# Performance work log

Measured on AMD Instinct MI355X. Metric: run time of the kernel, lower is better.

Reference implementation:

```python
import jax, jax.numpy as jnp
import numpy as np

D = 300      # dim_in (hardcoded in HGConv)
N_CAT = 3    # n_categories
M = 16384    # nodes
E = 4096     # hyperedges


def setup_inputs() -> dict:
    key = jax.random.key(0)
    ks = jax.random.split(key, 11)
    s = 1.0 / np.sqrt(D)
    u = lambda k, shape: jax.random.uniform(k, shape, jnp.float32, -s, s)
    return {
        "node_feats": jax.random.normal(ks[0], (M, D), jnp.float32),
        "edge_feats": jax.random.normal(ks[1], (E, D), jnp.float32),
        "inc_mat": jax.random.uniform(ks[2], (M, E), jnp.float32),
        # VertexConv params (Linear weights stored as (in, out); torch stores transpose)
        "W_att": u(ks[3], (D, D)),       # attention, no bias
        "W_proj": u(ks[4], (D, D)),      # projection, no bias
        "alpha": jnp.array(0.5, jnp.float32),
        # HypergraphEdgeAggregation params
        "ec_W_att": u(ks[5], (D, 1)),    # attention, no bias
        "ec_W_proj": u(ks[6], (D, D)),
        "ec_b_proj": u(ks[7], (D,)),
        # final classifier
        "fc_W": u(ks[8], (D, N_CAT)),
        "fc_b": u(ks[9], (N_CAT,)),
    }


def reference(node_feats, edge_feats, inc_mat, W_att, W_proj, alpha,
              ec_W_att, ec_W_proj, ec_b_proj, fc_W, fc_b):
    # --- VertexConv ---
    # edge attention scores: inc^T @ (X @ W_att)  -> (e, d)
    edge_att = inc_mat.T @ (node_feats @ W_att)
    attn = jax.nn.softmax(edge_att, axis=1)
    # fused equivalent of einsum('me,md->med') then einsum('med,ed->ed'):
    # edge_feat[e,d] = (inc^T @ X)[e,d] * attn[e,d]
    ef = (inc_mat.T @ node_feats) * attn
    ef = ef @ W_proj
    ef = alpha * edge_feats + (1.0 - alpha) * ef          # residual mix
    # --- HypergraphEdgeAggregation ---
    scores = ef @ ec_W_att                                # (e, 1)
    w = jax.nn.softmax(scores, axis=0)                    # softmax over edges
    pooled = jnp.sum(ef * w, axis=0)                      # (d,)
    out = pooled @ ec_W_proj + ec_b_proj                  # (d,)
    # --- classifier (LogSoftmax is defined but NOT applied in forward) ---
    logits = out @ fc_W + fc_b                            # (n_categories,)
    return logits
```

## Files before the change

### kernel.cpp

```cpp
#include <hip/hip_runtime.h>
#include <math.h>

typedef _Float16 f16;
typedef _Float16 f16x8 __attribute__((ext_vector_type(8)));
typedef _Float16 f16x4 __attribute__((ext_vector_type(4)));
typedef __fp16 fp16x2 __attribute__((ext_vector_type(2)));
typedef float f32x4 __attribute__((ext_vector_type(4)));
typedef float f32x16 __attribute__((ext_vector_type(16)));

#define NM 16384
#define NE 4096
#define ND 300
#define DP 320
#define PS 1310720

__device__ __forceinline__ int swz(int r) { return (r ^ (r >> 2)) & 3; }

#define GLOAD_LDS16(gsrc, ldst)                                              \
  __builtin_amdgcn_global_load_lds(                                          \
      (__attribute__((address_space(1))) void*)(gsrc),                       \
      (__attribute__((address_space(3))) void*)(ldst), 16, 0, 0)

__global__ __launch_bounds__(256) void k01_prep(const float* __restrict__ X,
                                                const float* __restrict__ Watt,
                                                f16* __restrict__ XT,
                                                f16* __restrict__ WT) {
  __shared__ f16 tile[64][324];
  const int bx = blockIdx.x;
  if (bx < 256) {
    int m0 = bx * 64;
    for (int idx = threadIdx.x; idx < 64 * 80; idx += 256) {
      int m = idx / 80, q = idx % 80;
      int d = q * 4;
      float4 v = make_float4(0.f, 0.f, 0.f, 0.f);
      if (d < ND) v = *(const float4*)(X + (size_t)(m0 + m) * ND + d);
      tile[m][d] = (f16)v.x; tile[m][d + 1] = (f16)v.y;
      tile[m][d + 2] = (f16)v.z; tile[m][d + 3] = (f16)v.w;
    }
    __syncthreads();
    for (int idx = threadIdx.x; idx < DP * 8; idx += 256) {
      int d = idx >> 3, part = idx & 7;
      f16x8 hv;
#pragma unroll
      for (int i = 0; i < 8; ++i) hv[i] = tile[part * 8 + i][d];
      *(f16x8*)(XT + (size_t)d * NM + m0 + part * 8) = hv;
    }
  } else {
    int idx = (bx - 256) * 256 + threadIdx.x;
    if (idx < DP * DP) {
      int j = idx / DP, d = idx % DP;
      float v = (j < ND && d < ND) ? Watt[d * ND + j] : 0.f;
      WT[(size_t)j * DP + d] = (f16)v;
    }
  }
}

#define K2WAIT(N) asm volatile("s_waitcnt vmcnt(" #N ") lgkmcnt(0)" ::: "memory")
#define K2BAR()                                        \
  do {                                                 \
    asm volatile("" ::: "memory");                     \
    __builtin_amdgcn_s_barrier();                      \
    asm volatile("" ::: "memory");                     \
  } while (0)

__global__ __launch_bounds__(256, 2) void k2_bigmm(const float* __restrict__ inc,
                                                   const f16* __restrict__ XT,
                                                   f16* __restrict__ Zp) {
  __shared__ __align__(16) char lds[57344];
  const int t = threadIdx.x, lane = t & 63, wid = t >> 6;
  const int bx = blockIdx.x;
  const int kb = (bx & 7) | (((bx >> 3) & 1) << 3);
  const int eb = bx >> 4;
  const int e0 = eb * 128;
  const size_t kbase = (size_t)kb * 1024;
  f16* __restrict__ Zout = Zp + (size_t)kb * PS;

  const int we = wid >> 1, wj = wid & 1;
  const int l31 = lane & 31, oct = lane >> 5;
  int sl[2];
#pragma unroll
  for (int kk = 0; kk < 2; ++kk)
    sl[kk] = (((kk * 2 + oct) ^ ((l31 >> 1) & 3)) & 3) << 4;
  const int arow = (we * 64 + l31) * 64;
  const int brow = (wj * 160 + l31) * 64;
  const int ep = t & 63, kq = t >> 6;
  const int sA = (kq ^ ((ep >> 1) & 3)) & 3;
  const int wa0 = 40960 + ep * 64 + sA * 16;
  const int wa1 = 40960 + (ep + 64) * 64 + sA * 16;
  const float* pA = inc + (kbase + kq * 8) * NE + e0 + ep;
  const int br = wid * 80 + (lane >> 2);
  const f16* pB = XT + (size_t)br * NM + kbase + 8 * ((lane & 3) ^ ((lane >> 3) & 3));

  float rAx0[8], rAy0[8], rAx1[8], rAy1[8];
  f32x16 acc[2][5];
#pragma unroll
  for (int me = 0; me < 2; ++me)
#pragma unroll
    for (int f = 0; f < 5; ++f)
#pragma unroll
      for (int r = 0; r < 16; ++r) acc[me][f][r] = 0.f;

#define LOADA(RX, RY)                                                          \
  {                                                                            \
    _Pragma("unroll") for (int i = 0; i < 8; ++i) {                            \
      RX[i] = pA[(size_t)i * NE];                                              \
      RY[i] = pA[(size_t)i * NE + 64];                                         \
    }                                                                          \
    pA += (size_t)32 * NE;                                                     \
  }
#define DMAB(S)                                                                \
  {                                                                            \
    _Pragma("unroll") for (int i = 0; i < 5; ++i) {                            \
      GLOAD_LDS16(pB + (size_t)(i * 16) * NM,                                  \
                  lds + (S)*20480 + wid * 5120 + i * 1024);                    \
    }                                                                          \
    pB += 32;                                                                  \
  }
#define WRITEA(RX, RY, S)                                                      \
  {                                                                            \
    union { fp16x2 h; uint32_t u; } ux_[4], uy_[4];                            \
    _Pragma("unroll") for (int z = 0; z < 4; ++z) {                            \
      ux_[z].h = __builtin_amdgcn_cvt_pkrtz(RX[2 * z], RX[2 * z + 1]);         \
      uy_[z].h = __builtin_amdgcn_cvt_pkrtz(RY[2 * z], RY[2 * z + 1]);         \
    }                                                                          \
    *(uint4*)(lds + wa0 + (S)*8192) =                                          \
        make_uint4(ux_[0].u, ux_[1].u, ux_[2].u, ux_[3].u);                    \
    *(uint4*)(lds + wa1 + (S)*8192) =                                          \
        make_uint4(uy_[0].u, uy_[1].u, uy_[2].u, uy_[3].u);                    \
  }
#define COMPUTE(S)                                                             \
  {                                                                            \
    __builtin_amdgcn_s_setprio(1);                                             \
    _Pragma("unroll") for (int kk = 0; kk < 2; ++kk) {                         \
      f16x8 a0_ = *(const f16x8*)(lds + 40960 + (S)*8192 + arow + sl[kk]);     \
      f16x8 a1_ = *(const f16x8*)(lds + 40960 + (S)*8192 + arow + 2048 + sl[kk]); \
      _Pragma("unroll") for (int f = 0; f < 5; ++f) {                          \
        f16x8 b_ = *(const f16x8*)(lds + (S)*20480 + brow + f * 2048 + sl[kk]); \
        acc[0][f] = __builtin_amdgcn_mfma_f32_32x32x16_f16(a0_, b_, acc[0][f], 0, 0, 0); \
        acc[1][f] = __builtin_amdgcn_mfma_f32_32x32x16_f16(a1_, b_, acc[1][f], 0, 0, 0); \
      }                                                                        \
    }                                                                          \
    __builtin_amdgcn_s_setprio(0);                                             \
  }

  LOADA(rAx0, rAy0);
  DMAB(0);
  WRITEA(rAx0, rAy0, 0);
  LOADA(rAx0, rAy0);
  DMAB(1);
  K2WAIT(21);
  K2BAR();

  for (int it = 0; it < 15; ++it) {
    COMPUTE(0);
    K2BAR();
    LOADA(rAx1, rAy1);
    DMAB(0);
    WRITEA(rAx0, rAy0, 1);
    K2WAIT(21);
    K2BAR();
    COMPUTE(1);
    K2BAR();
    LOADA(rAx0, rAy0);
    DMAB(1);
    WRITEA(rAx1, rAy1, 0);
    K2WAIT(21);
    K2BAR();
  }
  COMPUTE(0);
  K2BAR();
  WRITEA(rAx0, rAy0, 1);
  K2WAIT(0);
  K2BAR();
  COMPUTE(1);

#pragma unroll
  for (int me = 0; me < 2; ++me)
#pragma unroll
    for (int f = 0; f < 5; ++f) {
      int jg = wj * 160 + f * 32 + l31;
      int ebase = e0 + we * 64 + me * 32 + 4 * oct;
#pragma unroll
      for (int r = 0; r < 16; ++r) {
        int eg = ebase + (r & 3) + 8 * (r >> 2);
        Zout[(size_t)eg * DP + jg] = (f16)acc[me][f][r];
      }
    }
#undef LOADA
#undef DMAB
#undef WRITEA
}

__global__ __launch_bounds__(256) void k2s_sum(const f16* __restrict__ Zp,
                                               f16* __restrict__ EF0) {
  const int idx = (blockIdx.x * 256 + threadIdx.x) * 4;
  float s0 = 0.f, s1 = 0.f, s2 = 0.f, s3 = 0.f;
#pragma unroll
  for (int i = 0; i < 16; ++i) {
    f16x4 v = *(const f16x4*)(Zp + (size_t)i * PS + idx);
    s0 += (float)v[0]; s1 += (float)v[1]; s2 += (float)v[2]; s3 += (float)v[3];
  }
  f16x4 o;
  o[0] = (f16)s0; o[1] = (f16)s1; o[2] = (f16)s2; o[3] = (f16)s3;
  *(f16x4*)(EF0 + idx) = o;
}

__global__ __launch_bounds__(256, 1) void k2b_att(const f16* __restrict__ EF0,
                                                  const f16* __restrict__ WT,
                                                  float* __restrict__ att) {
  constexpr int STEPS = 10;
  __shared__ __align__(16) char lds[57344];
  const int t = threadIdx.x, lane = t & 63, wid = t >> 6;
  const int e0 = blockIdx.x * 128;
  const int we = wid >> 1, wj = wid & 1;
  const int l31 = lane & 31, oct = lane >> 5;
  int sl[2];
#pragma unroll
  for (int kk = 0; kk < 2; ++kk)
    sl[kk] = (((kk * 2 + oct) ^ ((l31 >> 1) & 3)) & 3) << 4;
  const int arow = (we * 64 + l31) * 64;
  const int brow = (wj * 160 + l31) * 64;
  const int srcsw = 8 * ((lane & 3) ^ ((lane >> 3) & 3));
  const f16* pA = EF0 + (size_t)(e0 + wid * 32 + (lane >> 2)) * DP + srcsw;
  const f16* pB = WT + (size_t)(wid * 80 + (lane >> 2)) * DP + srcsw;

  f32x16 acc[2][5];
#pragma unroll
  for (int me = 0; me < 2; ++me)
#pragma unroll
    for (int f = 0; f < 5; ++f)
#pragma unroll
      for (int r = 0; r < 16; ++r) acc[me][f][r] = 0.f;

#define STAGE2(S)                                                              \
  {                                                                            \
    _Pragma("unroll") for (int i = 0; i < 2; ++i) {                            \
      GLOAD_LDS16(pA + (size_t)(i * 16) * DP,                                  \
                  lds + 40960 + (S)*8192 + wid * 2048 + i * 1024);             \
    }                                                                          \
    pA += 32;                                                                  \
    _Pragma("unroll") for (int i = 0; i < 5; ++i) {                            \
      GLOAD_LDS16(pB + (size_t)(i * 16) * DP,                                  \
                  lds + (S)*20480 + wid * 5120 + i * 1024);                    \
    }                                                                          \
    pB += 32;                                                                  \
  }

  STAGE2(0);
  STAGE2(1);
  K2WAIT(7);
  K2BAR();
  for (int tt = 0; tt < STEPS - 2; ++tt) {
    COMPUTE(tt & 1);
    K2BAR();
    STAGE2(tt & 1);
    K2WAIT(7);
    K2BAR();
  }
  COMPUTE(0);
  K2BAR();
  K2WAIT(0);
  COMPUTE(1);

#pragma unroll
  for (int me = 0; me < 2; ++me)
#pragma unroll
    for (int f = 0; f < 5; ++f) {
      int jg = wj * 160 + f * 32 + l31;
      int ebase = e0 + we * 64 + me * 32 + 4 * oct;
#pragma unroll
      for (int r = 0; r < 16; ++r) {
        int eg = ebase + (r & 3) + 8 * (r >> 2);
        att[(size_t)eg * DP + jg] = acc[me][f][r];
      }
    }
#undef STAGE2
#undef COMPUTE
}

__global__ __launch_bounds__(256) void k3_edge(const float* __restrict__ att,
                                               const f16* __restrict__ EF0,
                                               const float* __restrict__ edge_feats,
                                               const float* __restrict__ Wproj,
                                               const float* __restrict__ alphaP,
                                               const float* __restrict__ ecWatt,
                                               float* __restrict__ ef,
                                               float* __restrict__ scores) {
  __shared__ float efw[16][304];
  const int t = threadIdx.x, lane = t & 63, w = t >> 6;
  const int e0 = blockIdx.x * 16;
  for (int el = 0; el < 4; ++el) {
    int e = e0 + w * 4 + el;
    const size_t ro = (size_t)e * DP;
    float p[5];
    float mx = -1e30f;
#pragma unroll
    for (int u = 0; u < 5; ++u) {
      int d = u * 64 + lane;
      p[u] = (d < ND) ? att[ro + d] : -1e30f;
      mx = fmaxf(mx, p[u]);
    }
    for (int o = 32; o; o >>= 1) mx = fmaxf(mx, __shfl_xor(mx, o));
    float s = 0.f;
#pragma unroll
    for (int u = 0; u < 5; ++u) {
      int d = u * 64 + lane;
      float pe = (d < ND) ? expf(p[u] - mx) : 0.f;
      p[u] = pe;
      s += pe;
    }
    for (int o = 32; o; o >>= 1) s += __shfl_xor(s, o);
    float inv = 1.f / s;
#pragma unroll
    for (int u = 0; u < 5; ++u) {
      int d = u * 64 + lane;
      if (d < 304)
        efw[w * 4 + el][d] = (d < ND) ? (float)EF0[ro + d] * p[u] * inv : 0.f;
    }
  }
  __syncthreads();
  const int jl = lane & 15, kc = lane >> 4;
  const float alpha = alphaP[0];
  float acc[4][19];
#pragma unroll
  for (int ei = 0; ei < 4; ++ei)
#pragma unroll
    for (int jj = 0; jj < 19; ++jj) acc[ei][jj] = 0.f;
  const int d0 = kc * 75;
  const float* efw0 = &efw[w * 4 + 0][0];
  const float* efw1 = &efw[w * 4 + 1][0];
  const float* efw2 = &efw[w * 4 + 2][0];
  const float* efw3 = &efw[w * 4 + 3][0];
  for (int dd = 0; dd < 75; ++dd) {
    int d = d0 + dd;
    const float* wr = Wproj + (size_t)d * ND + jl;
    float w0 = efw0[d], w1 = efw1[d], w2 = efw2[d], w3 = efw3[d];
#pragma unroll
    for (int jj = 0; jj < 19; ++jj) {
      int j = jl + jj * 16;
      float wv = (j < ND) ? wr[jj * 16] : 0.f;
      acc[0][jj] += w0 * wv;
      acc[1][jj] += w1 * wv;
      acc[2][jj] += w2 * wv;
      acc[3][jj] += w3 * wv;
    }
  }
#pragma unroll
  for (int ei = 0; ei < 4; ++ei)
#pragma unroll
    for (int jj = 0; jj < 19; ++jj) {
      acc[ei][jj] += __shfl_xor(acc[ei][jj], 16);
      acc[ei][jj] += __shfl_xor(acc[ei][jj], 32);
    }
  float scp[4] = {0.f, 0.f, 0.f, 0.f};
#pragma unroll
  for (int ei = 0; ei < 4; ++ei) {
    int e = e0 + w * 4 + ei;
#pragma unroll
    for (int jj = 0; jj < 19; ++jj) {
      int j = jl + jj * 16;
      float v = 0.f;
      if (j < ND) {
        v = alpha * edge_feats[(size_t)e * ND + j] + (1.f - alpha) * acc[ei][jj];
        scp[ei] += v * ecWatt[j];
      }
      if (kc == 0) ef[(size_t)e * 304 + j] = v;
    }
  }
#pragma unroll
  for (int ei = 0; ei < 4; ++ei)
    for (int o = 8; o; o >>= 1) scp[ei] += __shfl_xor(scp[ei], o);
  if (lane == 0) {
#pragma unroll
    for (int ei = 0; ei < 4; ++ei) scores[e0 + w * 4 + ei] = scp[ei];
  }
}

__global__ __launch_bounds__(256) void k4ab_pool(const float* __restrict__ sc,
                                                 const float* __restrict__ ef,
                                                 float* __restrict__ pp) {
  __shared__ float redm[4];
  __shared__ float reds[4];
  __shared__ float wsh[64];
  const int t = threadIdx.x, lane = t & 63, w = t >> 6;
  float v[16];
  float mx = -1e30f;
#pragma unroll
  for (int u = 0; u < 16; ++u) {
    v[u] = sc[t + u * 256];
    mx = fmaxf(mx, v[u]);
  }
  for (int o = 32; o; o >>= 1) mx = fmaxf(mx, __shfl_xor(mx, o));
  if (lane == 0) redm[w] = mx;
  __syncthreads();
  float m2 = fmaxf(fmaxf(redm[0], redm[1]), fmaxf(redm[2], redm[3]));
  float s = 0.f;
#pragma unroll
  for (int u = 0; u < 16; ++u) s += expf(v[u] - m2);
  for (int o = 32; o; o >>= 1) s += __shfl_xor(s, o);
  if (lane == 0) reds[w] = s;
  __syncthreads();
  float inv = 1.f / (reds[0] + reds[1] + reds[2] + reds[3]);
  const int e0 = blockIdx.x * 64;
  if (t < 64) wsh[t] = expf(sc[e0 + t] - m2) * inv;
  __syncthreads();
  for (int j = t; j < 304; j += 256) {
    float acc = 0.f;
#pragma unroll 8
    for (int e = 0; e < 64; ++e) acc += wsh[e] * ef[(size_t)(e0 + e) * 304 + j];
    pp[blockIdx.x * 304 + j] = acc;
  }
}

__global__ __launch_bounds__(320) void k4c_final(const float* __restrict__ pp,
                                                 const float* __restrict__ ecWp,
                                                 const float* __restrict__ ecb,
                                                 const float* __restrict__ fcW,
                                                 const float* __restrict__ fcb,
                                                 float* __restrict__ out) {
  __shared__ float pooled[304];
  __shared__ float o[304];
  const int t = threadIdx.x;
  if (t < 304) {
    float acc = 0.f;
#pragma unroll 8
    for (int b = 0; b < 64; ++b) acc += pp[b * 304 + t];
    pooled[t] = acc;
  }
  __syncthreads();
  if (t < ND) {
    float acc = ecb[t];
#pragma unroll 4
    for (int j = 0; j < ND; ++j) acc += pooled[j] * ecWp[(size_t)j * ND + t];
    o[t] = acc;
  }
  __syncthreads();
  if (t < 64) {
#pragma unroll
    for (int c = 0; c < 3; ++c) {
      float a = 0.f;
      for (int j2 = t; j2 < ND; j2 += 64) a += o[j2] * fcW[j2 * 3 + c];
      for (int off = 32; off; off >>= 1) a += __shfl_xor(a, off);
      if (t == 0) out[c] = a + fcb[c];
    }
  }
}

extern "C" void kernel_launch(void* const* d_in, const int* in_sizes, int n_in,
                              void* d_out, int out_size, void* d_ws, size_t ws_size,
                              hipStream_t stream) {
  const float* X = (const float*)d_in[0];
  const float* EFEATS = (const float*)d_in[1];
  const float* INC = (const float*)d_in[2];
  const float* WATT = (const float*)d_in[3];
  const float* WPROJ = (const float*)d_in[4];
  const float* ALPHA = (const float*)d_in[5];
  const float* ECATT = (const float*)d_in[6];
  const float* ECWP = (const float*)d_in[7];
  const float* ECB = (const float*)d_in[8];
  const float* FCW = (const float*)d_in[9];
  const float* FCB = (const float*)d_in[10];

  char* ws = (char*)d_ws;
  f16* XT = (f16*)(ws);
  f16* Zp = (f16*)(ws + 10485760);
  f16* WT = (f16*)(ws + 52428800);
  f16* EF0 = (f16*)(ws + 52633600);
  float* att = (float*)(ws + 55255040);
  float* ef = (float*)(ws + 60497920);
  float* sc = (float*)(ws + 65478656);
  float* pp = (float*)(ws + 65495040);

  hipLaunchKernelGGL(k01_prep, dim3(656), dim3(256), 0, stream, X, WATT, XT, WT);
  hipLaunchKernelGGL(k2_bigmm, dim3(512), dim3(256), 0, stream, INC, XT, Zp);
  hipLaunchKernelGGL(k2s_sum, dim3(1280), dim3(256), 0, stream, Zp, EF0);
  hipLaunchKernelGGL(k2b_att, dim3(32), dim3(256), 0, stream, EF0, WT, att);
  hipLaunchKernelGGL(k3_edge, dim3(256), dim3(256), 0, stream, att, EF0, EFEATS,
                     WPROJ, ALPHA, ECATT, ef, sc);
  hipLaunchKernelGGL(k4ab_pool, dim3(64), dim3(256), 0, stream, sc, ef, pp);
  hipLaunchKernelGGL(k4c_final, dim3(1), dim3(320), 0, stream, pp, ECWP, ECB, FCW,
                     FCB, (float*)d_out);
}
```

Before: 245.1 us.

## Triple-buffer big GEMM B tiles, vectorize A loads, fuse split-K sum into attention GEMM

```diff
diff --git a/kernel.cpp b/kernel.cpp
--- a/kernel.cpp
+++ b/kernel.cpp
@@ -14,12 +14,24 @@
 #define DP 320
 #define PS 1310720
 
-__device__ __forceinline__ int swz(int r) { return (r ^ (r >> 2)) & 3; }
-
 #define GLOAD_LDS16(gsrc, ldst)                                              \
   __builtin_amdgcn_global_load_lds(                                          \
       (__attribute__((address_space(1))) void*)(gsrc),                       \
       (__attribute__((address_space(3))) void*)(ldst), 16, 0, 0)
+
+#define K2WAIT(N) asm volatile("s_waitcnt vmcnt(" #N ") lgkmcnt(0)" ::: "memory")
+#define K2BAR()                                        \
+  do {                                                 \
+    asm volatile("" ::: "memory");                     \
+    __builtin_amdgcn_s_barrier();                      \
+    asm volatile("" ::: "memory");                     \
+  } while (0)
+#define K2BARW()                                       \
+  do {                                                 \
+    asm volatile("s_waitcnt lgkmcnt(0)" ::: "memory"); \
+    __builtin_amdgcn_s_barrier();                      \
+    asm volatile("" ::: "memory");                     \
+  } while (0)
 
 __global__ __launch_bounds__(256) void k01_prep(const float* __restrict__ X,
                                                 const float* __restrict__ Watt,
@@ -55,18 +67,10 @@
   }
 }
 
-#define K2WAIT(N) asm volatile("s_waitcnt vmcnt(" #N ") lgkmcnt(0)" ::: "memory")
-#define K2BAR()                                        \
-  do {                                                 \
-    asm volatile("" ::: "memory");                     \
-    __builtin_amdgcn_s_barrier();                      \
-    asm volatile("" ::: "memory");                     \
-  } while (0)
-
 __global__ __launch_bounds__(256, 2) void k2_bigmm(const float* __restrict__ inc,
                                                    const f16* __restrict__ XT,
                                                    f16* __restrict__ Zp) {
-  __shared__ __align__(16) char lds[57344];
+  __shared__ __align__(16) char lds[77824];
   const int t = threadIdx.x, lane = t & 63, wid = t >> 6;
   const int bx = blockIdx.x;
   const int kb = (bx & 7) | (((bx >> 3) & 1) << 3);
@@ -84,14 +88,13 @@
   const int arow = (we * 64 + l31) * 64;
   const int brow = (wj * 160 + l31) * 64;
   const int ep = t & 63, kq = t >> 6;
-  const int sA = (kq ^ ((ep >> 1) & 3)) & 3;
-  const int wa0 = 40960 + ep * 64 + sA * 16;
-  const int wa1 = 40960 + (ep + 64) * 64 + sA * 16;
-  const float* pA = inc + (kbase + kq * 8) * NE + e0 + ep;
+  const int sA = (kq ^ (ep & 3)) & 3;
+  const int wa0 = 61440 + ep * 128 + sA * 16;
+  const float* pA = inc + (kbase + kq * 8) * NE + e0 + 2 * ep;
   const int br = wid * 80 + (lane >> 2);
   const f16* pB = XT + (size_t)br * NM + kbase + 8 * ((lane & 3) ^ ((lane >> 3) & 3));
 
-  float rAx0[8], rAy0[8], rAx1[8], rAy1[8];
+  float2 rA0[8], rA1[8];
   f32x16 acc[2][5];
 #pragma unroll
   for (int me = 0; me < 2; ++me)
@@ -100,12 +103,10 @@
 #pragma unroll
       for (int r = 0; r < 16; ++r) acc[me][f][r] = 0.f;
 
-#define LOADA(RX, RY)                                                          \
-  {                                                                            \
-    _Pragma("unroll") for (int i = 0; i < 8; ++i) {                            \
-      RX[i] = pA[(size_t)i * NE];                                              \
-      RY[i] = pA[(size_t)i * NE + 64];                                         \
-    }                                                                          \
+#define LOADA(R)                                                               \
+  {                                                                            \
+    _Pragma("unroll") for (int i = 0; i < 8; ++i)                              \
+        R[i] = *(const float2*)(pA + (size_t)i * NE);                          \
     pA += (size_t)32 * NE;                                                     \
   }
 #define DMAB(S)                                                                \
@@ -116,63 +117,66 @@
     }                                                                          \
     pB += 32;                                                                  \
   }
-#define WRITEA(RX, RY, S)                                                      \
+#define WRITEA(R, S)                                                           \
   {                                                                            \
     union { fp16x2 h; uint32_t u; } ux_[4], uy_[4];                            \
     _Pragma("unroll") for (int z = 0; z < 4; ++z) {                            \
-      ux_[z].h = __builtin_amdgcn_cvt_pkrtz(RX[2 * z], RX[2 * z + 1]);         \
-      uy_[z].h = __builtin_amdgcn_cvt_pkrtz(RY[2 * z], RY[2 * z + 1]);         \
+      ux_[z].h = __builtin_amdgcn_cvt_pkrtz(R[2 * z].x, R[2 * z + 1].x);       \
+      uy_[z].h = __builtin_amdgcn_cvt_pkrtz(R[2 * z].y, R[2 * z + 1].y);       \
     }                                                                          \
     *(uint4*)(lds + wa0 + (S)*8192) =                                          \
         make_uint4(ux_[0].u, ux_[1].u, ux_[2].u, ux_[3].u);                    \
-    *(uint4*)(lds + wa1 + (S)*8192) =                                          \
+    *(uint4*)(lds + wa0 + 64 + (S)*8192) =                                     \
         make_uint4(uy_[0].u, uy_[1].u, uy_[2].u, uy_[3].u);                    \
   }
-#define COMPUTE(S)                                                             \
+#define COMPUTE(BS, AS)                                                        \
   {                                                                            \
     __builtin_amdgcn_s_setprio(1);                                             \
     _Pragma("unroll") for (int kk = 0; kk < 2; ++kk) {                         \
-      f16x8 a0_ = *(const f16x8*)(lds + 40960 + (S)*8192 + arow + sl[kk]);     \
-      f16x8 a1_ = *(const f16x8*)(lds + 40960 + (S)*8192 + arow + 2048 + sl[kk]); \
+      f16x8 a0_ = *(const f16x8*)(lds + 61440 + (AS)*8192 + arow + sl[kk]);    \
+      f16x8 a1_ = *(const f16x8*)(lds + 61440 + (AS)*8192 + arow + 2048 + sl[kk]); \
       _Pragma("unroll") for (int f = 0; f < 5; ++f) {                          \
-        f16x8 b_ = *(const f16x8*)(lds + (S)*20480 + brow + f * 2048 + sl[kk]); \
+        f16x8 b_ = *(const f16x8*)(lds + (BS)*20480 + brow + f * 2048 + sl[kk]); \
         acc[0][f] = __builtin_amdgcn_mfma_f32_32x32x16_f16(a0_, b_, acc[0][f], 0, 0, 0); \
         acc[1][f] = __builtin_amdgcn_mfma_f32_32x32x16_f16(a1_, b_, acc[1][f], 0, 0, 0); \
       }                                                                        \
     }                                                                          \
     __builtin_amdgcn_s_setprio(0);                                             \
   }
-
-  LOADA(rAx0, rAy0);
+#define BODY(BSTG, BCMP, AW, AC, RL, RW)                                       \
+  DMAB(BSTG);                                                                  \
+  LOADA(RL);                                                                   \
+  WRITEA(RW, AW); \
+  K2BARW();                                                                    \
+  COMPUTE(BCMP, AC);                                                           \
+  K2BAR();
+
+  LOADA(rA0);
   DMAB(0);
-  WRITEA(rAx0, rAy0, 0);
-  LOADA(rAx0, rAy0);
+  WRITEA(rA0, 0);
+  LOADA(rA1);
   DMAB(1);
-  K2WAIT(21);
-  K2BAR();
-
-  for (int it = 0; it < 15; ++it) {
-    COMPUTE(0);
-    K2BAR();
-    LOADA(rAx1, rAy1);
-    DMAB(0);
-    WRITEA(rAx0, rAy0, 1);
-    K2WAIT(21);
-    K2BAR();
-    COMPUTE(1);
-    K2BAR();
-    LOADA(rAx0, rAy0);
-    DMAB(1);
-    WRITEA(rAx1, rAy1, 0);
-    K2WAIT(21);
-    K2BAR();
-  }
-  COMPUTE(0);
-  K2BAR();
-  WRITEA(rAx0, rAy0, 1);
+  BODY(2, 0, 1, 0, rA0, rA1);
+
+  for (int it = 0; it < 4; ++it) {
+    BODY(0, 1, 0, 1, rA1, rA0);
+    BODY(1, 2, 1, 0, rA0, rA1);
+    BODY(2, 0, 0, 1, rA1, rA0);
+    BODY(0, 1, 1, 0, rA0, rA1);
+    BODY(1, 2, 0, 1, rA1, rA0);
+    BODY(2, 0, 1, 0, rA0, rA1);
+  }
+  BODY(0, 1, 0, 1, rA1, rA0);
+  BODY(1, 2, 1, 0, rA0, rA1);
+  BODY(2, 0, 0, 1, rA1, rA0);
+  BODY(0, 1, 1, 0, rA0, rA1);
+  BODY(1, 2, 0, 1, rA1, rA0);
+  WRITEA(rA1, 1);
   K2WAIT(0);
   K2BAR();
-  COMPUTE(1);
+  COMPUTE(0, 0);
+  K2BAR();
+  COMPUTE(1, 1);
 
 #pragma unroll
   for (int me = 0; me < 2; ++me)
@@ -189,55 +193,59 @@
 #undef LOADA
 #undef DMAB
 #undef WRITEA
-}
-
-__global__ __launch_bounds__(256) void k2s_sum(const f16* __restrict__ Zp,
-                                               f16* __restrict__ EF0) {
-  const int idx = (blockIdx.x * 256 + threadIdx.x) * 4;
-  float s0 = 0.f, s1 = 0.f, s2 = 0.f, s3 = 0.f;
-#pragma unroll
-  for (int i = 0; i < 16; ++i) {
-    f16x4 v = *(const f16x4*)(Zp + (size_t)i * PS + idx);
-    s0 += (float)v[0]; s1 += (float)v[1]; s2 += (float)v[2]; s3 += (float)v[3];
-  }
-  f16x4 o;
-  o[0] = (f16)s0; o[1] = (f16)s1; o[2] = (f16)s2; o[3] = (f16)s3;
-  *(f16x4*)(EF0 + idx) = o;
-}
-
-__global__ __launch_bounds__(256, 1) void k2b_att(const f16* __restrict__ EF0,
-                                                  const f16* __restrict__ WT,
-                                                  float* __restrict__ att) {
-  constexpr int STEPS = 10;
-  __shared__ __align__(16) char lds[57344];
+#undef COMPUTE
+#undef BODY
+}
+
+__global__ __launch_bounds__(256, 1) void k2bs_att(const f16* __restrict__ Zp,
+                                                   const f16* __restrict__ WT,
+                                                   f16* __restrict__ EF0,
+                                                   float* __restrict__ att) {
+  __shared__ __align__(16) char lds[49152];
   const int t = threadIdx.x, lane = t & 63, wid = t >> 6;
-  const int e0 = blockIdx.x * 128;
+  const int e0 = blockIdx.x * 64;
+  {
+    const size_t base = (size_t)e0 * DP;
+    for (int i = t; i < 2560; i += 256) {
+      size_t idx = base + (size_t)i * 8;
+      float s[8];
+#pragma unroll
+      for (int z = 0; z < 8; ++z) s[z] = 0.f;
+#pragma unroll
+      for (int p = 0; p < 16; ++p) {
+        f16x8 v = *(const f16x8*)(Zp + (size_t)p * PS + idx);
+#pragma unroll
+        for (int z = 0; z < 8; ++z) s[z] += (float)v[z];
+      }
+      f16x8 o;
+#pragma unroll
+      for (int z = 0; z < 8; ++z) o[z] = (f16)s[z];
+      *(f16x8*)(EF0 + idx) = o;
+    }
+    asm volatile("s_waitcnt vmcnt(0)" ::: "memory");
+    __syncthreads();
+  }
   const int we = wid >> 1, wj = wid & 1;
   const int l31 = lane & 31, oct = lane >> 5;
   int sl[2];
 #pragma unroll
   for (int kk = 0; kk < 2; ++kk)
     sl[kk] = (((kk * 2 + oct) ^ ((l31 >> 1) & 3)) & 3) << 4;
-  const int arow = (we * 64 + l31) * 64;
+  const int arow = (we * 32 + l31) * 64;
   const int brow = (wj * 160 + l31) * 64;
   const int srcsw = 8 * ((lane & 3) ^ ((lane >> 3) & 3));
-  const f16* pA = EF0 + (size_t)(e0 + wid * 32 + (lane >> 2)) * DP + srcsw;
+  const f16* pA = EF0 + (size_t)(e0 + wid * 16 + (lane >> 2)) * DP + srcsw;
   const f16* pB = WT + (size_t)(wid * 80 + (lane >> 2)) * DP + srcsw;
 
-  f32x16 acc[2][5];
-#pragma unroll
-  for (int me = 0; me < 2; ++me)
-#pragma unroll
-    for (int f = 0; f < 5; ++f)
-#pragma unroll
-      for (int r = 0; r < 16; ++r) acc[me][f][r] = 0.f;
+  f32x16 acc[5];
+#pragma unroll
+  for (int f = 0; f < 5; ++f)
+#pragma unroll
+    for (int r = 0; r < 16; ++r) acc[f][r] = 0.f;
 
 #define STAGE2(S)                                                              \
   {                                                                            \
-    _Pragma("unroll") for (int i = 0; i < 2; ++i) {                            \
-      GLOAD_LDS16(pA + (size_t)(i * 16) * DP,                                  \
-                  lds + 40960 + (S)*8192 + wid * 2048 + i * 1024);             \
-    }                                                                          \
+    GLOAD_LDS16(pA, lds + 40960 + (S)*4096 + wid * 1024);                      \
     pA += 32;                                                                  \
     _Pragma("unroll") for (int i = 0; i < 5; ++i) {                            \
       GLOAD_LDS16(pB + (size_t)(i * 16) * DP,                                  \
@@ -245,37 +253,45 @@
     }                                                                          \
     pB += 32;                                                                  \
   }
+#define COMPUTE2(S)                                                            \
+  {                                                                            \
+    _Pragma("unroll") for (int kk = 0; kk < 2; ++kk) {                         \
+      f16x8 a_ = *(const f16x8*)(lds + 40960 + (S)*4096 + arow + sl[kk]);      \
+      _Pragma("unroll") for (int f = 0; f < 5; ++f) {                          \
+        f16x8 b_ = *(const f16x8*)(lds + (S)*20480 + brow + f * 2048 + sl[kk]); \
+        acc[f] = __builtin_amdgcn_mfma_f32_32x32x16_f16(a_, b_, acc[f], 0, 0, 0); \
+      }                                                                        \
+    }                                                                          \
+  }
 
   STAGE2(0);
   STAGE2(1);
-  K2WAIT(7);
+  K2WAIT(6);
   K2BAR();
-  for (int tt = 0; tt < STEPS - 2; ++tt) {
-    COMPUTE(tt & 1);
+  for (int tt = 0; tt < 8; ++tt) {
+    COMPUTE2(tt & 1);
     K2BAR();
     STAGE2(tt & 1);
-    K2WAIT(7);
+    K2WAIT(6);
     K2BAR();
   }
-  COMPUTE(0);
+  COMPUTE2(0);
   K2BAR();
   K2WAIT(0);
-  COMPUTE(1);
-
-#pragma unroll
-  for (int me = 0; me < 2; ++me)
-#pragma unroll
-    for (int f = 0; f < 5; ++f) {
-      int jg = wj * 160 + f * 32 + l31;
-      int ebase = e0 + we * 64 + me * 32 + 4 * oct;
-#pragma unroll
-      for (int r = 0; r < 16; ++r) {
-        int eg = ebase + (r & 3) + 8 * (r >> 2);
-        att[(size_t)eg * DP + jg] = acc[me][f][r];
-      }
-    }
+  COMPUTE2(1);
+
+#pragma unroll
+  for (int f = 0; f < 5; ++f) {
+    int jg = wj * 160 + f * 32 + l31;
+    int ebase = e0 + we * 32 + 4 * oct;
+#pragma unroll
+    for (int r = 0; r < 16; ++r) {
+      int eg = ebase + (r & 3) + 8 * (r >> 2);
+      att[(size_t)eg * DP + jg] = acc[f][r];
+    }
+  }
 #undef STAGE2
-#undef COMPUTE
+#undef COMPUTE2
 }
 
 __global__ __launch_bounds__(256) void k3_edge(const float* __restrict__ att,
@@ -473,8 +489,7 @@
 
   hipLaunchKernelGGL(k01_prep, dim3(656), dim3(256), 0, stream, X, WATT, XT, WT);
   hipLaunchKernelGGL(k2_bigmm, dim3(512), dim3(256), 0, stream, INC, XT, Zp);
-  hipLaunchKernelGGL(k2s_sum, dim3(1280), dim3(256), 0, stream, Zp, EF0);
-  hipLaunchKernelGGL(k2b_att, dim3(32), dim3(256), 0, stream, EF0, WT, att);
+  hipLaunchKernelGGL(k2bs_att, dim3(64), dim3(256), 0, stream, Zp, WT, EF0, att);
   hipLaunchKernelGGL(k3_edge, dim3(256), dim3(256), 0, stream, att, EF0, EFEATS,
                      WPROJ, ALPHA, ECATT, ef, sc);
   hipLaunchKernelGGL(k4ab_pool, dim3(64), dim3(256), 0, stream, sc, ef, pp);
```

Result: no change. 242.6 us (-1.0%).
